# Kernel tuning notes

Measured on AMD Instinct MI355X. Metric: run time of the kernel, lower is better.

The kernel has to match this reference:

```python
import jax, jax.numpy as jnp
import numpy as np

FAN_IN, FAN_MID, FAN_OUT = 512, 256, 40
N_NODES, N_EDGES = 50000, 800000
LN_EPS = 1e-5


def gcn_conv(x, edge_index, W, b, num_nodes):
    # h = X W  (transform before aggregate; fan_out < fan_in)
    h = x @ W  # [N, F_out]
    src, dst = edge_index[0], edge_index[1]
    loop = jnp.arange(num_nodes, dtype=src.dtype)
    src = jnp.concatenate([src, loop])
    dst = jnp.concatenate([dst, loop])
    # symmetric normalization D^{-1/2} (A+I) D^{-1/2}
    deg = jax.ops.segment_sum(jnp.ones_like(dst, dtype=h.dtype), dst,
                              num_segments=num_nodes)  # includes self-loop -> >= 1
    dinv = deg ** -0.5
    norm = dinv[src] * dinv[dst]  # [E+N]
    msg = h[src] * norm[:, None]  # [E+N, F_out]  (largest intermediate)
    out = jax.ops.segment_sum(msg, dst, num_segments=num_nodes)
    return out + b


def layer_norm(x, gamma, beta):
    mu = jnp.mean(x, axis=-1, keepdims=True)
    var = jnp.var(x, axis=-1, keepdims=True)
    return (x - mu) * jax.lax.rsqrt(var + LN_EPS) * gamma + beta


def setup_inputs() -> dict:
    key = jax.random.key(0)
    ks = jax.random.split(key, 8)
    x = jax.random.normal(ks[0], (N_NODES, FAN_IN), dtype=jnp.float32)
    edge_index = jax.random.randint(ks[1], (2, N_EDGES), 0, N_NODES, dtype=jnp.int64)
    W1 = jax.random.normal(ks[2], (FAN_IN, FAN_MID), dtype=jnp.float32) / np.sqrt(FAN_IN)
    b1 = jnp.zeros((FAN_MID,), dtype=jnp.float32)
    g1 = jnp.ones((FAN_MID,), dtype=jnp.float32)
    be1 = jnp.zeros((FAN_MID,), dtype=jnp.float32)
    W2 = jax.random.normal(ks[3], (FAN_MID, FAN_OUT), dtype=jnp.float32) / np.sqrt(FAN_MID)
    b2 = jnp.zeros((FAN_OUT,), dtype=jnp.float32)
    g2 = jnp.ones((FAN_OUT,), dtype=jnp.float32)
    be2 = jnp.zeros((FAN_OUT,), dtype=jnp.float32)
    return {"x": x, "edge_index": edge_index, "W1": W1, "b1": b1, "g1": g1,
            "be1": be1, "W2": W2, "b2": b2, "g2": g2, "be2": be2}


def reference(x, edge_index, W1, b1, g1, be1, W2, b2, g2, be2):
    n = x.shape[0]
    h = jax.nn.elu(layer_norm(gcn_conv(x, edge_index, W1, b1, n), g1, be1))
    # dropout is identity in eval mode
    h = jax.nn.elu(layer_norm(gcn_conv(h, edge_index, W2, b2, n), g2, be2))
    return jax.nn.log_softmax(h, axis=1)
```

## Files before the change

### kernel.cpp

```cpp
#include <hip/hip_runtime.h>
#include <math.h>

#define NN 50000
#define NE 800000
#define F_IN 512
#define F_MID 256
#define F_OUT 40
#define LN_EPS 1e-5f
#define NRT 3125
#define H2S 64
#define CAP 48

typedef float f32x4 __attribute__((ext_vector_type(4)));
typedef short s16x8 __attribute__((ext_vector_type(8)));
typedef unsigned short ushort;

__device__ __forceinline__ short f2bf(float f) {
    unsigned u = __float_as_uint(f);
    return (short)((u + 0x7FFF + ((u >> 16) & 1)) >> 16);
}
__device__ __forceinline__ float bf2f(ushort u) {
    return __uint_as_float(((unsigned)u) << 16);
}

__global__ void k_init(const float* __restrict__ W1, const float* __restrict__ W2,
                       short* __restrict__ B1p, short* __restrict__ B2p,
                       int* __restrict__ cnt) {
    int bid = blockIdx.x;
    if (bid < 512) {
        int idx = bid * 256 + threadIdx.x;
        int j = idx & 7;
        int l = (idx >> 3) & 63;
        int ks = (idx >> 9) & 15;
        int n = idx >> 13;
        int k = ks * 32 + (l >> 4) * 8 + j;
        int col = n * 16 + (l & 15);
        B1p[idx] = f2bf(W1[k * F_MID + col]);
    } else if (bid < 560) {
        int idx = (bid - 512) * 256 + threadIdx.x;
        int j = idx & 7;
        int l = (idx >> 3) & 63;
        int ks = (idx >> 9) & 7;
        int n = idx >> 12;
        int k = ks * 32 + (l >> 4) * 8 + j;
        int col = n * 16 + (l & 15);
        B2p[idx] = (col < F_OUT) ? f2bf(W2[k * F_OUT + col]) : (short)0;
    } else {
        int i = (bid - 560) * 256 + threadIdx.x;
        if (i < NN) cnt[i] = 0;
    }
}

__global__ void k_fillF(const int* __restrict__ ei, int* __restrict__ cnt,
                        int* __restrict__ esrcF) {
    int e = blockIdx.x * 256 + threadIdx.x;
    if (e >= NE) return;
    int src = ei[e];
    int dst = ei[NE + e];
    int pos = atomicAdd(&cnt[dst], 1);
    if (pos < CAP) esrcF[dst * CAP + pos] = src;
}

__global__ __launch_bounds__(256) void k_castX(const float* __restrict__ X,
                                               const int* __restrict__ cnt,
                                               ushort* __restrict__ Xp) {
    int rt = blockIdx.x;
    int t = threadIdx.x;
#pragma unroll
    for (int i = 0; i < 4; ++i) {
        int s = t + i * 256;
        int ks = s >> 6, lane = s & 63;
        int lm = lane & 15, kg = lane >> 4;
        int row = rt * 16 + lm;
        float sc = rsqrtf((float)(cnt[row] + 1));
        const float4* src = (const float4*)&X[(size_t)row * F_IN + ks * 32 + kg * 8];
        float4 a = src[0], b = src[1];
        s16x8 pk;
        pk[0] = f2bf(a.x * sc); pk[1] = f2bf(a.y * sc);
        pk[2] = f2bf(a.z * sc); pk[3] = f2bf(a.w * sc);
        pk[4] = f2bf(b.x * sc); pk[5] = f2bf(b.y * sc);
        pk[6] = f2bf(b.z * sc); pk[7] = f2bf(b.w * sc);
        *(s16x8*)&Xp[((size_t)(rt * 16 + ks) * 64 + lane) * 8] = pk;
    }
}

__global__ __launch_bounds__(256) void k_gemm1m(const ushort* __restrict__ Xp,
                                                const short* __restrict__ B1p,
                                                ushort* __restrict__ H) {
    int t = threadIdx.x;
    int w = t >> 6, lane = t & 63;
    int lm = lane & 15, kg = lane >> 4;
    int rt0 = blockIdx.x * 4 + (w >> 1) * 2;
    int nb = (w & 1) * 8;
    const s16x8* xp = (const s16x8*)Xp;
    const s16x8* bp = (const s16x8*)B1p;
    bool rok[2] = { rt0 < NRT, rt0 + 1 < NRT };

    f32x4 acc[2][8];
#pragma unroll
    for (int m = 0; m < 2; ++m)
#pragma unroll
        for (int n = 0; n < 8; ++n) acc[m][n] = (f32x4){0.f, 0.f, 0.f, 0.f};

#pragma unroll
    for (int ks = 0; ks < 16; ++ks) {
        s16x8 af[2];
#pragma unroll
        for (int m = 0; m < 2; ++m)
            af[m] = rok[m] ? xp[(size_t)((rt0 + m) * 16 + ks) * 64 + lane] : (s16x8)0;
        s16x8 bfr[8];
#pragma unroll
        for (int n = 0; n < 8; ++n)
            bfr[n] = bp[(size_t)((nb + n) * 16 + ks) * 64 + lane];
#pragma unroll
        for (int m = 0; m < 2; ++m)
#pragma unroll
            for (int n = 0; n < 8; ++n)
                acc[m][n] = __builtin_amdgcn_mfma_f32_16x16x32_bf16(af[m], bfr[n], acc[m][n], 0, 0, 0);
    }

#pragma unroll
    for (int m = 0; m < 2; ++m) {
        if (!rok[m]) continue;
#pragma unroll
        for (int reg = 0; reg < 4; ++reg) {
            int row = (rt0 + m) * 16 + kg * 4 + reg;
#pragma unroll
            for (int n = 0; n < 8; ++n)
                H[(size_t)row * F_MID + (nb + n) * 16 + lm] = (ushort)f2bf(acc[m][n][reg]);
        }
    }
}

__global__ __launch_bounds__(256) void k_agg1(const int* __restrict__ cnt,
                                              const int* __restrict__ esrcF,
                                              const ushort* __restrict__ H,
                                              const float* __restrict__ b,
                                              const float* __restrict__ g,
                                              const float* __restrict__ be,
                                              ushort* __restrict__ O,
                                              int off) {
    int node = off + blockIdx.x * 4 + (threadIdx.x >> 6);
    if (node >= NN) return;
    int lane = threadIdx.x & 63;
    int c = lane * 4;
    ushort4 sv = *(const ushort4*)&H[(size_t)node * F_MID + c];
    float a0 = bf2f(sv.x), a1 = bf2f(sv.y), a2 = bf2f(sv.z), a3 = bf2f(sv.w);
    int cntv = cnt[node];
    int deg = cntv < CAP ? cntv : CAP;
    const int* nbl = esrcF + node * CAP;
    int j = 0;
    for (; j + 3 < deg; j += 4) {
        int s0 = nbl[j], s1 = nbl[j + 1], s2 = nbl[j + 2], s3 = nbl[j + 3];
        ushort4 v0 = *(const ushort4*)&H[(size_t)s0 * F_MID + c];
        ushort4 v1 = *(const ushort4*)&H[(size_t)s1 * F_MID + c];
        ushort4 v2 = *(const ushort4*)&H[(size_t)s2 * F_MID + c];
        ushort4 v3 = *(const ushort4*)&H[(size_t)s3 * F_MID + c];
        a0 += bf2f(v0.x) + bf2f(v1.x) + bf2f(v2.x) + bf2f(v3.x);
        a1 += bf2f(v0.y) + bf2f(v1.y) + bf2f(v2.y) + bf2f(v3.y);
        a2 += bf2f(v0.z) + bf2f(v1.z) + bf2f(v2.z) + bf2f(v3.z);
        a3 += bf2f(v0.w) + bf2f(v1.w) + bf2f(v2.w) + bf2f(v3.w);
    }
    for (; j < deg; ++j) {
        int s0 = nbl[j];
        ushort4 v0 = *(const ushort4*)&H[(size_t)s0 * F_MID + c];
        a0 += bf2f(v0.x); a1 += bf2f(v0.y); a2 += bf2f(v0.z); a3 += bf2f(v0.w);
    }
    float s = rsqrtf((float)(cntv + 1));
    float v0 = s * a0 + b[c + 0];
    float v1 = s * a1 + b[c + 1];
    float v2 = s * a2 + b[c + 2];
    float v3 = s * a3 + b[c + 3];
    float sum = v0 + v1 + v2 + v3;
    float sq = v0 * v0 + v1 * v1 + v2 * v2 + v3 * v3;
#pragma unroll
    for (int o = 32; o; o >>= 1) {
        sum += __shfl_xor(sum, o, 64);
        sq  += __shfl_xor(sq, o, 64);
    }
    float mu = sum * (1.0f / F_MID);
    float var = sq * (1.0f / F_MID) - mu * mu;
    float rstd = rsqrtf(var + LN_EPS);
    float y0 = (v0 - mu) * rstd * g[c + 0] + be[c + 0];
    float y1 = (v1 - mu) * rstd * g[c + 1] + be[c + 1];
    float y2 = (v2 - mu) * rstd * g[c + 2] + be[c + 2];
    float y3 = (v3 - mu) * rstd * g[c + 3] + be[c + 3];
    ushort4 o4;
    o4.x = (ushort)f2bf(y0 > 0.f ? y0 : expm1f(y0));
    o4.y = (ushort)f2bf(y1 > 0.f ? y1 : expm1f(y1));
    o4.z = (ushort)f2bf(y2 > 0.f ? y2 : expm1f(y2));
    o4.w = (ushort)f2bf(y3 > 0.f ? y3 : expm1f(y3));
    *(ushort4*)&O[(size_t)node * F_MID + c] = o4;
}

__global__ __launch_bounds__(256) void k_gemm2m(const ushort* __restrict__ Hin,
                                                const short* __restrict__ B2p,
                                                const int* __restrict__ cnt,
                                                ushort* __restrict__ H2) {
    int t = threadIdx.x;
    int wv = t >> 6, lane = t & 63;
    int lm = lane & 15, kg = lane >> 4;
    int r0 = blockIdx.x * 128 + wv * 32;

    const s16x8* ap[2];
    bool rok[2];
#pragma unroll
    for (int m = 0; m < 2; ++m) {
        int row = r0 + m * 16 + lm;
        rok[m] = row < NN;
        ap[m] = (const s16x8*)(Hin + (size_t)row * F_MID + kg * 8);
    }
    const s16x8* bp = (const s16x8*)B2p;

    f32x4 acc[2][3];
#pragma unroll
    for (int m = 0; m < 2; ++m)
#pragma unroll
        for (int n = 0; n < 3; ++n) acc[m][n] = (f32x4){0.f, 0.f, 0.f, 0.f};

#pragma unroll
    for (int ks = 0; ks < 8; ++ks) {
        s16x8 af[2];
#pragma unroll
        for (int m = 0; m < 2; ++m)
            af[m] = rok[m] ? ap[m][ks * 4] : (s16x8)0;
        s16x8 bfr[3];
#pragma unroll
        for (int n = 0; n < 3; ++n)
            bfr[n] = bp[(size_t)(n * 8 + ks) * 64 + lane];
#pragma unroll
        for (int m = 0; m < 2; ++m)
#pragma unroll
            for (int n = 0; n < 3; ++n)
                acc[m][n] = __builtin_amdgcn_mfma_f32_16x16x32_bf16(af[m], bfr[n], acc[m][n], 0, 0, 0);
    }

#pragma unroll
    for (int m = 0; m < 2; ++m) {
#pragma unroll
        for (int reg = 0; reg < 4; ++reg) {
            int row = r0 + m * 16 + kg * 4 + reg;
            if (row < NN) {
                float s = rsqrtf((float)(cnt[row] + 1));
#pragma unroll
                for (int n = 0; n < 3; ++n)
                    H2[(size_t)row * H2S + n * 16 + lm] = (ushort)f2bf(acc[m][n][reg] * s);
            }
        }
    }
}

__global__ __launch_bounds__(256) void k_agg2(const int* __restrict__ cnt,
                                              const int* __restrict__ esrcF,
                                              const ushort* __restrict__ H2,
                                              const float* __restrict__ b,
                                              const float* __restrict__ g,
                                              const float* __restrict__ be,
                                              float* __restrict__ out) {
    __shared__ float sm[4][8][52];
    int wv = threadIdx.x >> 6;
    int node = blockIdx.x * 4 + wv;
    int lane = threadIdx.x & 63;
    int gsl = lane >> 3;
    int c8 = (lane & 7) * 8;
    bool ld = c8 < 48;
    int cntv = cnt[node];
    int deg = cntv < CAP ? cntv : CAP;
    const int* nbl = esrcF + node * CAP;
    float acc[8] = {0.f, 0.f, 0.f, 0.f, 0.f, 0.f, 0.f, 0.f};
    if (gsl == 0 && ld) {
        s16x8 v = *(const s16x8*)&H2[(size_t)node * H2S + c8];
#pragma unroll
        for (int i = 0; i < 8; ++i) acc[i] = bf2f((ushort)v[i]);
    }
    for (int j = gsl; j < deg; j += 8) {
        if (ld) {
            int s = nbl[j];
            s16x8 v = *(const s16x8*)&H2[(size_t)s * H2S + c8];
#pragma unroll
            for (int i = 0; i < 8; ++i) acc[i] += bf2f((ushort)v[i]);
        }
    }
    if (ld) {
#pragma unroll
        for (int i = 0; i < 8; ++i) sm[wv][gsl][c8 + i] = acc[i];
    }
    __syncthreads();

    bool av = lane < F_OUT;
    float v = 0.f;
    if (av) {
        float tot = 0.f;
#pragma unroll
        for (int gg = 0; gg < 8; ++gg) tot += sm[wv][gg][lane];
        v = rsqrtf((float)(cntv + 1)) * tot + b[lane];
    }
    float sum = v, sq = v * v;
#pragma unroll
    for (int o = 32; o; o >>= 1) {
        sum += __shfl_xor(sum, o, 64);
        sq  += __shfl_xor(sq, o, 64);
    }
    float mu = sum * (1.0f / F_OUT);
    float var = sq * (1.0f / F_OUT) - mu * mu;
    float rstd = rsqrtf(var + LN_EPS);
    float y = av ? ((v - mu) * rstd * g[lane] + be[lane]) : 0.f;
    float el = y > 0.f ? y : expm1f(y);
    float mx = av ? el : -INFINITY;
#pragma unroll
    for (int o = 32; o; o >>= 1) mx = fmaxf(mx, __shfl_xor(mx, o, 64));
    float ex = av ? expf(el - mx) : 0.f;
    float se = ex;
#pragma unroll
    for (int o = 32; o; o >>= 1) se += __shfl_xor(se, o, 64);
    if (av) out[(size_t)node * F_OUT + lane] = el - mx - logf(se);
}

extern "C" void kernel_launch(void* const* d_in, const int* in_sizes, int n_in,
                              void* d_out, int out_size, void* d_ws, size_t ws_size,
                              hipStream_t stream) {
    const float* x   = (const float*)d_in[0];
    const int*   ei  = (const int*)d_in[1];
    const float* W1  = (const float*)d_in[2];
    const float* b1  = (const float*)d_in[3];
    const float* g1  = (const float*)d_in[4];
    const float* be1 = (const float*)d_in[5];
    const float* W2  = (const float*)d_in[6];
    const float* b2  = (const float*)d_in[7];
    const float* g2  = (const float*)d_in[8];
    const float* be2 = (const float*)d_in[9];
    float* out = (float*)d_out;

    char* p = (char*)d_ws;
    ushort* h1p = (ushort*)p;           p += (size_t)NN * F_MID * 2;
    ushort* h2p = (ushort*)d_ws;
    ushort* h1  = (ushort*)p;           p += (size_t)NN * F_MID * 2;
    short* B1p  = (short*)p;            p += (size_t)F_MID * F_IN * 2;
    short* B2p  = (short*)p;            p += 48 * 256 * 2;
    int* cnt    = (int*)p;              p += NN * 4;
    int* esrcF  = (int*)p;              p += (size_t)NN * CAP * 4;
    ushort* Xp  = (ushort*)p;

    k_init<<<560 + 196, 256, 0, stream>>>(W1, W2, B1p, B2p, cnt);
    k_fillF<<<(NE + 255) / 256, 256, 0, stream>>>(ei, cnt, esrcF);
    k_castX<<<NRT, 256, 0, stream>>>(x, cnt, Xp);

    k_gemm1m<<<(NRT + 3) / 4, 256, 0, stream>>>(Xp, B1p, h1p);
    k_agg1<<<6250, 256, 0, stream>>>(cnt, esrcF, h1p, b1, g1, be1, h1, 0);
    k_agg1<<<6250, 256, 0, stream>>>(cnt, esrcF, h1p, b1, g1, be1, h1, 25000);
    k_gemm2m<<<(NN + 127) / 128, 256, 0, stream>>>(h1, B2p, cnt, h2p);
    k_agg2<<<NN / 4, 256, 0, stream>>>(cnt, esrcF, h2p, b2, g2, be2, out);
}
```

Before: 219.2 us.

## Fuse X cast into GEMM1, store neighbor indices as ushort, merge agg1 launches

Removes the separate k_castX pass. k_gemm1m now loads fp32 X directly, applies the degree scaling and converts to bf16 in registers, so the bf16 copy of X is never written to or read back from global memory. Neighbor source indices are stored as 16-bit values, which fit because node ids stay below 65536, halving index traffic in fill and both aggregations. The two half-range k_agg1 launches become one. The cost is that the GEMM now does more uncoalesced fp32 loads and conversion work inside its inner loop.

```diff
diff --git a/kernel.cpp b/kernel.cpp
--- a/kernel.cpp
+++ b/kernel.cpp
@@ -52,39 +52,17 @@
 }
 
 __global__ void k_fillF(const int* __restrict__ ei, int* __restrict__ cnt,
-                        int* __restrict__ esrcF) {
+                        ushort* __restrict__ esrcF) {
     int e = blockIdx.x * 256 + threadIdx.x;
     if (e >= NE) return;
     int src = ei[e];
     int dst = ei[NE + e];
     int pos = atomicAdd(&cnt[dst], 1);
-    if (pos < CAP) esrcF[dst * CAP + pos] = src;
-}
-
-__global__ __launch_bounds__(256) void k_castX(const float* __restrict__ X,
-                                               const int* __restrict__ cnt,
-                                               ushort* __restrict__ Xp) {
-    int rt = blockIdx.x;
-    int t = threadIdx.x;
-#pragma unroll
-    for (int i = 0; i < 4; ++i) {
-        int s = t + i * 256;
-        int ks = s >> 6, lane = s & 63;
-        int lm = lane & 15, kg = lane >> 4;
-        int row = rt * 16 + lm;
-        float sc = rsqrtf((float)(cnt[row] + 1));
-        const float4* src = (const float4*)&X[(size_t)row * F_IN + ks * 32 + kg * 8];
-        float4 a = src[0], b = src[1];
-        s16x8 pk;
-        pk[0] = f2bf(a.x * sc); pk[1] = f2bf(a.y * sc);
-        pk[2] = f2bf(a.z * sc); pk[3] = f2bf(a.w * sc);
-        pk[4] = f2bf(b.x * sc); pk[5] = f2bf(b.y * sc);
-        pk[6] = f2bf(b.z * sc); pk[7] = f2bf(b.w * sc);
-        *(s16x8*)&Xp[((size_t)(rt * 16 + ks) * 64 + lane) * 8] = pk;
-    }
-}
-
-__global__ __launch_bounds__(256) void k_gemm1m(const ushort* __restrict__ Xp,
+    if (pos < CAP) esrcF[dst * CAP + pos] = (ushort)src;
+}
+
+__global__ __launch_bounds__(256) void k_gemm1m(const float* __restrict__ X,
+                                                const int* __restrict__ cnt,
                                                 const short* __restrict__ B1p,
                                                 ushort* __restrict__ H) {
     int t = threadIdx.x;
@@ -92,9 +70,19 @@
     int lm = lane & 15, kg = lane >> 4;
     int rt0 = blockIdx.x * 4 + (w >> 1) * 2;
     int nb = (w & 1) * 8;
-    const s16x8* xp = (const s16x8*)Xp;
     const s16x8* bp = (const s16x8*)B1p;
-    bool rok[2] = { rt0 < NRT, rt0 + 1 < NRT };
+
+    const float4* ap[2];
+    float sc[2];
+    bool rok[2];
+#pragma unroll
+    for (int m = 0; m < 2; ++m) {
+        int rt = rt0 + m;
+        rok[m] = rt < NRT;
+        int row = (rok[m] ? rt : 0) * 16 + lm;
+        ap[m] = (const float4*)(X + (size_t)row * F_IN + kg * 8);
+        sc[m] = rok[m] ? rsqrtf((float)(cnt[row] + 1)) : 0.f;
+    }
 
     f32x4 acc[2][8];
 #pragma unroll
@@ -106,8 +94,17 @@
     for (int ks = 0; ks < 16; ++ks) {
         s16x8 af[2];
 #pragma unroll
-        for (int m = 0; m < 2; ++m)
-            af[m] = rok[m] ? xp[(size_t)((rt0 + m) * 16 + ks) * 64 + lane] : (s16x8)0;
+        for (int m = 0; m < 2; ++m) {
+            float4 a = ap[m][ks * 8];
+            float4 b = ap[m][ks * 8 + 1];
+            float s = sc[m];
+            s16x8 pk;
+            pk[0] = f2bf(a.x * s); pk[1] = f2bf(a.y * s);
+            pk[2] = f2bf(a.z * s); pk[3] = f2bf(a.w * s);
+            pk[4] = f2bf(b.x * s); pk[5] = f2bf(b.y * s);
+            pk[6] = f2bf(b.z * s); pk[7] = f2bf(b.w * s);
+            af[m] = pk;
+        }
         s16x8 bfr[8];
 #pragma unroll
         for (int n = 0; n < 8; ++n)
@@ -133,14 +130,13 @@
 }
 
 __global__ __launch_bounds__(256) void k_agg1(const int* __restrict__ cnt,
-                                              const int* __restrict__ esrcF,
+                                              const ushort* __restrict__ esrcF,
                                               const ushort* __restrict__ H,
                                               const float* __restrict__ b,
                                               const float* __restrict__ g,
                                               const float* __restrict__ be,
-                                              ushort* __restrict__ O,
-                                              int off) {
-    int node = off + blockIdx.x * 4 + (threadIdx.x >> 6);
+                                              ushort* __restrict__ O) {
+    int node = blockIdx.x * 4 + (threadIdx.x >> 6);
     if (node >= NN) return;
     int lane = threadIdx.x & 63;
     int c = lane * 4;
@@ -148,7 +144,7 @@
     float a0 = bf2f(sv.x), a1 = bf2f(sv.y), a2 = bf2f(sv.z), a3 = bf2f(sv.w);
     int cntv = cnt[node];
     int deg = cntv < CAP ? cntv : CAP;
-    const int* nbl = esrcF + node * CAP;
+    const ushort* nbl = esrcF + node * CAP;
     int j = 0;
     for (; j + 3 < deg; j += 4) {
         int s0 = nbl[j], s1 = nbl[j + 1], s2 = nbl[j + 2], s3 = nbl[j + 3];
@@ -251,7 +247,7 @@
 }
 
 __global__ __launch_bounds__(256) void k_agg2(const int* __restrict__ cnt,
-                                              const int* __restrict__ esrcF,
+                                              const ushort* __restrict__ esrcF,
                                               const ushort* __restrict__ H2,
                                               const float* __restrict__ b,
                                               const float* __restrict__ g,
@@ -266,7 +262,7 @@
     bool ld = c8 < 48;
     int cntv = cnt[node];
     int deg = cntv < CAP ? cntv : CAP;
-    const int* nbl = esrcF + node * CAP;
+    const ushort* nbl = esrcF + node * CAP;
     float acc[8] = {0.f, 0.f, 0.f, 0.f, 0.f, 0.f, 0.f, 0.f};
     if (gsl == 0 && ld) {
         s16x8 v = *(const s16x8*)&H2[(size_t)node * H2S + c8];
@@ -338,16 +334,12 @@
     short* B1p  = (short*)p;            p += (size_t)F_MID * F_IN * 2;
     short* B2p  = (short*)p;            p += 48 * 256 * 2;
     int* cnt    = (int*)p;              p += NN * 4;
-    int* esrcF  = (int*)p;              p += (size_t)NN * CAP * 4;
-    ushort* Xp  = (ushort*)p;
+    ushort* esrcF = (ushort*)p;
 
     k_init<<<560 + 196, 256, 0, stream>>>(W1, W2, B1p, B2p, cnt);
     k_fillF<<<(NE + 255) / 256, 256, 0, stream>>>(ei, cnt, esrcF);
-    k_castX<<<NRT, 256, 0, stream>>>(x, cnt, Xp);
-
-    k_gemm1m<<<(NRT + 3) / 4, 256, 0, stream>>>(Xp, B1p, h1p);
-    k_agg1<<<6250, 256, 0, stream>>>(cnt, esrcF, h1p, b1, g1, be1, h1, 0);
-    k_agg1<<<6250, 256, 0, stream>>>(cnt, esrcF, h1p, b1, g1, be1, h1, 25000);
+    k_gemm1m<<<(NRT + 3) / 4, 256, 0, stream>>>(x, cnt, B1p, h1p);
+    k_agg1<<<(NN + 3) / 4, 256, 0, stream>>>(cnt, esrcF, h1p, b1, g1, be1, h1);
     k_gemm2m<<<(NN + 127) / 128, 256, 0, stream>>>(h1, B2p, cnt, h2p);
     k_agg2<<<NN / 4, 256, 0, stream>>>(cnt, esrcF, h2p, b2, g2, be2, out);
 }
```

New measurement: 212.2 us. 1.03x faster.
